# Optimization experiments

Measured on AMD Instinct MI355X. Metric: run time of the kernel, lower is better.

Reference implementation:

```python
import jax, jax.numpy as jnp
import numpy as np

B, T, H, V = 64, 48, 512, 32000


def _uni(k, shape, fan_in):
    s = 1.0 / np.sqrt(fan_in)
    return jax.random.uniform(k, shape, jnp.float32, -s, s)


def setup_inputs() -> dict:
    key = jax.random.key(0)
    ks = jax.random.split(key, 21)
    inp = {
        "feat": jax.random.normal(ks[0], (B, T, H), jnp.float32),
        "caption": jax.random.normal(ks[1], (B, T, H), jnp.float32),
        "ids": jax.random.randint(ks[2], (B, T), 0, V),
    }
    i = 3
    for name, in_dim in (("1", H), ("2", 2 * H), ("d1", H), ("d2", 2 * H)):
        inp["w_ih" + name] = _uni(ks[i], (4 * H, in_dim), H); i += 1
        inp["w_hh" + name] = _uni(ks[i], (4 * H, H), H); i += 1
        inp["b_ih" + name] = _uni(ks[i], (4 * H,), H); i += 1
        inp["b_hh" + name] = _uni(ks[i], (4 * H,), H); i += 1
    inp["w_o"] = _uni(ks[i], (V, H), H); i += 1
    inp["b_o"] = _uni(ks[i], (V,), H)
    return inp


def lstm_cell(x, h, c, w_ih, w_hh, b_ih, b_hh):
    # PyTorch LSTMCell: gates in i, f, g, o order
    g = x @ w_ih.T + b_ih + h @ w_hh.T + b_hh
    gi, gf, gg, go = jnp.split(g, 4, axis=-1)
    c_new = jax.nn.sigmoid(gf) * c + jax.nn.sigmoid(gi) * jnp.tanh(gg)
    h_new = jax.nn.sigmoid(go) * jnp.tanh(c_new)
    return h_new, c_new


def reference(feat, caption, ids,
              w_ih1, w_hh1, b_ih1, b_hh1,
              w_ih2, w_hh2, b_ih2, b_hh2,
              w_ihd1, w_hhd1, b_ihd1, b_hhd1,
              w_ihd2, w_hhd2, b_ihd2, b_hhd2,
              w_o, b_o):
    pad = jnp.zeros((B, H), feat.dtype)
    z = jnp.zeros((B, H), feat.dtype)

    def enc_step(carry, x):
        h1, c1, h2, c2 = carry
        h1, c1 = lstm_cell(x, h1, c1, w_ih1, w_hh1, b_ih1, b_hh1)
        h2, c2 = lstm_cell(jnp.concatenate([pad, h1], 1), h2, c2,
                           w_ih2, w_hh2, b_ih2, b_hh2)
        return (h1, c1, h2, c2), None

    carry, _ = jax.lax.scan(enc_step, (z, z, z, z), jnp.swapaxes(feat, 0, 1))

    def dec_step(carry, xs):
        h1, c1, h2, c2 = carry
        cap, tgt = xs
        h1, c1 = lstm_cell(pad, h1, c1, w_ihd1, w_hhd1, b_ihd1, b_hhd1)
        h2, c2 = lstm_cell(jnp.concatenate([cap, h1], 1), h2, c2,
                           w_ihd2, w_hhd2, b_ihd2, b_hhd2)
        logits = h2 @ w_o.T + b_o  # [B, V]
        lp = jax.nn.log_softmax(logits, axis=-1)
        ce = -jnp.take_along_axis(lp, tgt[:, None], axis=1)[:, 0].mean()
        return (h1, c1, h2, c2), ce

    caps = jnp.swapaxes(caption[:, : T - 1, :], 0, 1)  # [T-1, B, H]
    tgts = jnp.swapaxes(ids[:, 1:T], 0, 1)             # [T-1, B]
    _, ces = jax.lax.scan(dec_step, carry, (caps, tgts))
    # total_loss += sum(mean_ce) / batch_size (word_loss is already a mean)
    return jnp.sum(ces) / B
```

## Files before the change

### kernel.cpp

```cpp
#include <hip/hip_runtime.h>
#include <math.h>

#define B_ 64
#define T_ 48
#define H_ 512
#define V_ 32000
#define G_ 2048
#define BH_ (B_*H_)
#define BG_ (B_*G_)

typedef short short8 __attribute__((ext_vector_type(8)));
typedef float f32x4 __attribute__((ext_vector_type(4)));

__device__ __forceinline__ float sigmoidf_(float x){ return 1.f/(1.f+__expf(-x)); }

__device__ __forceinline__ unsigned short f2bf(float f){
  unsigned u = __float_as_uint(f);
  u += 0x7fffu + ((u>>16)&1u);
  return (unsigned short)(u>>16);
}

__device__ __forceinline__ short8 cvt8(const float* g){
  float4 a = *(const float4*)g;
  float4 b = *(const float4*)(g+4);
  short8 v;
  v[0]=(short)f2bf(a.x); v[1]=(short)f2bf(a.y); v[2]=(short)f2bf(a.z); v[3]=(short)f2bf(a.w);
  v[4]=(short)f2bf(b.x); v[5]=(short)f2bf(b.y); v[6]=(short)f2bf(b.z); v[7]=(short)f2bf(b.w);
  return v;
}

#define F1_(i)   ((i)*16)
#define GO_(i)   ((32+(i))*16)
#define F2_(i)   ((96+(i))*16)
#define GO2_(i)  ((128+(i))*16)

__global__ void init_kernel(unsigned short* h1_0, unsigned short* h2_0, unsigned* flags){
  int i = blockIdx.x*256 + threadIdx.x;
  short8 z = {0,0,0,0,0,0,0,0};
  if (i < 4096) ((short8*)h1_0)[i] = z;
  else          ((short8*)h2_0)[i-4096] = z;
  if (i < 4096) flags[i] = 0u;
}

__global__ void cvt_cat_kernel(const float* __restrict__ s0, int ld0, int off0,
                               const float* __restrict__ s1, int ld1, int off1,
                               unsigned short* __restrict__ dst, int dld, long total8)
{
  int cols8 = dld >> 3;
  for (long i = blockIdx.x*256 + threadIdx.x; i < total8; i += (long)gridDim.x*256){
    int r = (int)(i / cols8);
    int k = (int)(i - (long)r*cols8) * 8;
    short8 v = (k < 512 || !s1) ? cvt8(s0 + (long)r*ld0 + off0 + k)
                                : cvt8(s1 + (long)r*ld1 + off1 + (k-512));
    *(short8*)(dst + (long)r*dld + k) = v;
  }
}

__global__ void bias_sum_kernel(const float* a1, const float* a2, float* o1,
                                const float* b1, const float* b2, float* o2){
  int n = blockIdx.x*256 + threadIdx.x;
  if (n < G_){ o1[n] = a1[n] + a2[n]; o2[n] = b1[n] + b2[n]; }
}

__global__ __launch_bounds__(512,1) void mm_pre_kernel(
    const float* __restrict__ A, int a_bstride,
    const unsigned short* __restrict__ Wbf,
    const float* __restrict__ bA, const float* __restrict__ bB,
    float* __restrict__ out)
{
  const int s = blockIdx.x, n0 = blockIdx.y*256;
  const int t = threadIdx.x, w = t>>6, l = t&63, ln = l&15, lk = l>>4;
  __shared__ short8 smA[64*64];
  __shared__ short8 smB[256*8];

  const float* af32 = A + (long)s*H_;

  f32x4 acc[4][2];
#pragma unroll
  for (int mf=0; mf<4; ++mf)
#pragma unroll
    for (int nf=0; nf<2; ++nf) acc[mf][nf] = (f32x4){0.f,0.f,0.f,0.f};

#pragma unroll
  for (int i=0;i<8;++i){ int e=i*4096+t*8; int m=e>>9, k=e&511;
    smA[m*64 + ((k>>3)^(m&7))] = cvt8(&af32[(long)m*a_bstride + k]); }

  for (int kc=0; kc<8; ++kc){
    __syncthreads();
#pragma unroll
    for (int i=0;i<4;++i){ int e=i*4096+t*8; int n=e>>6, k=e&63;
      smB[n*8 + ((k>>3)^(n&7))] = *(const short8*)(Wbf + (long)(n0+n)*512 + kc*64 + k); }
    __syncthreads();
#pragma unroll
    for (int ks2=0; ks2<2; ++ks2){
#pragma unroll
      for (int nf=0; nf<2; ++nf){
        int n = w*32 + nf*16 + ln;
        short8 bfr = smB[n*8 + ((ks2*4+lk)^(n&7))];
#pragma unroll
        for (int mf=0; mf<4; ++mf){
          int m = mf*16+ln;
          short8 afr = smA[m*64 + (((kc*2+ks2)*4+lk)^(m&7))];
          acc[mf][nf] = __builtin_amdgcn_mfma_f32_16x16x32_bf16(afr, bfr, acc[mf][nf], 0,0,0);
        }
      }
    }
  }
#pragma unroll
  for (int nf=0; nf<2; ++nf){
    int n = n0 + w*32 + nf*16 + ln;
    float bias = bA[n] + bB[n];
#pragma unroll
    for (int mf=0; mf<4; ++mf)
#pragma unroll
      for (int r=0; r<4; ++r){
        int m = mf*16 + lk*4 + r;
        out[(long)s*BG_ + (long)m*G_ + n] = acc[mf][nf][r] + bias;
      }
  }
}

__global__ __launch_bounds__(256,1) void fused_chain_kernel(
    const unsigned short* __restrict__ w1e, const unsigned short* __restrict__ w1d,
    const unsigned short* __restrict__ w2e, const unsigned short* __restrict__ w2d,
    const float* __restrict__ x1,
    const float* __restrict__ capq,
    const float* __restrict__ bd1s, const float* __restrict__ b2es,
    unsigned short* __restrict__ h1, unsigned short* __restrict__ h2,
    unsigned* __restrict__ flags)
{
  const int bc = blockIdx.x;
  const int isL2 = (bc >= 32);
  const int cb = bc & 31;
  const int t = threadIdx.x;
  const int wv = t>>6, l = t&63, ln = l&15, lk = l>>4;

  __shared__ short8 smA[64*128];
  __shared__ float gbuf[4][16][68];
  __shared__ float c_lds[16][68];
  unsigned short* stash = (unsigned short*)&smA[0];

  short8 W[32];
  const int col = wv*512 + cb*16 + ln;
  if (isL2){
    const long wrow = (long)col * 1024;
#pragma unroll
    for (int ks=0; ks<32; ++ks) W[ks] = *(const short8*)(w2e + wrow + ks*32 + lk*8);
  } else {
    const long wrow = (long)col * 512;
#pragma unroll
    for (int ks=0; ks<16; ++ks){
      W[ks]    = *(const short8*)(w1e + wrow + ks*32 + lk*8);
      W[16+ks] = *(const short8*)(w1d + wrow + ks*32 + lk*8);
    }
  }
  const float bext = isL2 ? b2es[col] : bd1s[col];

  for (int i=t; i<16*68; i+=256) (&c_lds[0][0])[i] = 0.f;
  __syncthreads();

  if (!isL2){
    for (int u=0; u<95; ++u){
      float prev[4][4];
      if (u < 48){
        const float* pp = x1 + (long)u*BG_ + col;
#pragma unroll
        for (int mf=0;mf<4;++mf)
#pragma unroll
          for (int r=0;r<4;++r) prev[mf][r] = pp[(long)(mf*16+lk*4+r)*G_];
      } else {
#pragma unroll
        for (int mf=0;mf<4;++mf)
#pragma unroll
          for (int r=0;r<4;++r) prev[mf][r] = bext;
      }
      { const unsigned short* hp = h1 + (long)u*BH_;
#pragma unroll
        for (int i=0;i<16;++i){ int e=i*2048+t*8; int m=e>>9, k=e&511;
          smA[m*128 + ((k>>3)^(m&7))] = *(const short8*)(hp + m*512 + k); } }
      __syncthreads();

      f32x4 acc[4];
#pragma unroll
      for (int mf=0;mf<4;++mf) acc[mf] = (f32x4){0.f,0.f,0.f,0.f};
      if (u < 48){
#pragma unroll
        for (int ks=0; ks<16; ++ks)
#pragma unroll
          for (int mf=0; mf<4; ++mf){
            int m = mf*16+ln;
            acc[mf] = __builtin_amdgcn_mfma_f32_16x16x32_bf16(
              smA[m*128 + ((ks*4+lk)^(m&7))], W[ks], acc[mf], 0,0,0);
          }
      } else {
#pragma unroll
        for (int ks=0; ks<16; ++ks)
#pragma unroll
          for (int mf=0; mf<4; ++mf){
            int m = mf*16+ln;
            acc[mf] = __builtin_amdgcn_mfma_f32_16x16x32_bf16(
              smA[m*128 + ((ks*4+lk)^(m&7))], W[16+ks], acc[mf], 0,0,0);
          }
      }
#pragma unroll
      for (int mf=0;mf<4;++mf)
#pragma unroll
        for (int r=0;r<4;++r) acc[mf][r] += prev[mf][r];

#pragma unroll
      for (int mf=0;mf<4;++mf) *(f32x4*)&gbuf[wv][ln][mf*16+lk*4] = acc[mf];
      __syncthreads();
      {
        int n = t&15, m0 = (t>>4)*4;
        float4 gi = *(float4*)&gbuf[0][n][m0];
        float4 gf = *(float4*)&gbuf[1][n][m0];
        float4 gg = *(float4*)&gbuf[2][n][m0];
        float4 go = *(float4*)&gbuf[3][n][m0];
        float4 c4 = *(float4*)&c_lds[n][m0];
        float cn[4];
        float a_i[4]={gi.x,gi.y,gi.z,gi.w}, a_f[4]={gf.x,gf.y,gf.z,gf.w};
        float a_g[4]={gg.x,gg.y,gg.z,gg.w}, a_o[4]={go.x,go.y,go.z,go.w};
        float ci[4]={c4.x,c4.y,c4.z,c4.w};
#pragma unroll
        for (int j=0;j<4;++j){
          float i_ = sigmoidf_(a_i[j]), f_ = sigmoidf_(a_f[j]), o_ = sigmoidf_(a_o[j]);
          float g_ = tanhf(a_g[j]);
          cn[j] = f_*ci[j] + i_*g_;
          stash[(m0+j)*24 + n] = f2bf(o_*tanhf(cn[j]));
        }
        *(float4*)&c_lds[n][m0] = make_float4(cn[0],cn[1],cn[2],cn[3]);
      }
      __syncthreads();
      {
        unsigned short* ho = h1 + (long)(u+1)*BH_ + cb*16;
        int m = t>>2, q = t&3;
        unsigned long long v = *(const unsigned long long*)&stash[m*24 + q*4];
        __hip_atomic_store((unsigned long long*)(ho + (long)m*512 + q*4), v,
                           __ATOMIC_RELAXED, __HIP_MEMORY_SCOPE_AGENT);
      }
      __syncthreads();

      {
        unsigned g = (unsigned)(u+1);
        if (t == 0)
          __hip_atomic_store(&flags[F1_(cb)], g, __ATOMIC_RELAXED, __HIP_MEMORY_SCOPE_AGENT);
        if (cb == 0){
          if (t < 32)
            while (__hip_atomic_load(&flags[F1_(t)], __ATOMIC_RELAXED, __HIP_MEMORY_SCOPE_AGENT) < g)
              __builtin_amdgcn_s_sleep(1);
          __syncthreads();
          if (t >= 1 && t < 64)
            __hip_atomic_store(&flags[GO_(t)], g, __ATOMIC_RELAXED, __HIP_MEMORY_SCOPE_AGENT);
        } else {
          if (u < 94){
            if (t == 0)
              while (__hip_atomic_load(&flags[GO_(cb)], __ATOMIC_RELAXED, __HIP_MEMORY_SCOPE_AGENT) < g)
                __builtin_amdgcn_s_sleep(1);
          }
          __syncthreads();
        }
      }
    }
  } else {
    for (int v=1; v<=95; ++v){
      if (v == 49){
        const long wrow = (long)col * 1024;
#pragma unroll
        for (int ks=0; ks<32; ++ks) W[ks] = *(const short8*)(w2d + wrow + ks*32 + lk*8);
      }
      int s2 = v-1;
      float prev[4][4];
      if (s2 < 48){
#pragma unroll
        for (int mf=0;mf<4;++mf)
#pragma unroll
          for (int r=0;r<4;++r) prev[mf][r] = bext;
      } else {
        const float* pp = capq + (long)(s2-48)*BG_ + col;
#pragma unroll
        for (int mf=0;mf<4;++mf)
#pragma unroll
          for (int r=0;r<4;++r) prev[mf][r] = pp[(long)(mf*16+lk*4+r)*G_];
      }

      if (t == 0){
        while (__hip_atomic_load(&flags[GO_(bc)], __ATOMIC_RELAXED, __HIP_MEMORY_SCOPE_AGENT) < (unsigned)v)
          __builtin_amdgcn_s_sleep(1);
      }
      __syncthreads();

      { const unsigned short* hpA = h2 + (long)(v-1)*BH_;
        const unsigned short* hpB = h1 + (long)v*BH_;
#pragma unroll
        for (int i=0;i<16;++i){ int e=i*2048+t*8; int m=e>>9, k=e&511;
          smA[m*128 + ((k>>3)^(m&7))]      = *(const short8*)(hpA + m*512 + k);
          smA[m*128 + ((k>>3)^(m&7)) + 64] = *(const short8*)(hpB + m*512 + k);
        } }
      __syncthreads();

      f32x4 acc[4];
#pragma unroll
      for (int mf=0;mf<4;++mf) acc[mf] = (f32x4){0.f,0.f,0.f,0.f};
#pragma unroll
      for (int ks=0; ks<32; ++ks)
#pragma unroll
        for (int mf=0; mf<4; ++mf){
          int m = mf*16+ln;
          acc[mf] = __builtin_amdgcn_mfma_f32_16x16x32_bf16(
            smA[m*128 + ((ks*4+lk)^(m&7))], W[ks], acc[mf], 0,0,0);
        }
#pragma unroll
      for (int mf=0;mf<4;++mf)
#pragma unroll
        for (int r=0;r<4;++r) acc[mf][r] += prev[mf][r];

#pragma unroll
      for (int mf=0;mf<4;++mf) *(f32x4*)&gbuf[wv][ln][mf*16+lk*4] = acc[mf];
      __syncthreads();
      {
        int n = t&15, m0 = (t>>4)*4;
        float4 gi = *(float4*)&gbuf[0][n][m0];
        float4 gf = *(float4*)&gbuf[1][n][m0];
        float4 gg = *(float4*)&gbuf[2][n][m0];
        float4 go = *(float4*)&gbuf[3][n][m0];
        float4 c4 = *(float4*)&c_lds[n][m0];
        float cn[4];
        float a_i[4]={gi.x,gi.y,gi.z,gi.w}, a_f[4]={gf.x,gf.y,gf.z,gf.w};
        float a_g[4]={gg.x,gg.y,gg.z,gg.w}, a_o[4]={go.x,go.y,go.z,go.w};
        float ci[4]={c4.x,c4.y,c4.z,c4.w};
#pragma unroll
        for (int j=0;j<4;++j){
          float i_ = sigmoidf_(a_i[j]), f_ = sigmoidf_(a_f[j]), o_ = sigmoidf_(a_o[j]);
          float g_ = tanhf(a_g[j]);
          cn[j] = f_*ci[j] + i_*g_;
          stash[(m0+j)*24 + n] = f2bf(o_*tanhf(cn[j]));
        }
        *(float4*)&c_lds[n][m0] = make_float4(cn[0],cn[1],cn[2],cn[3]);
      }
      __syncthreads();
      {
        unsigned short* ho = h2 + (long)v*BH_ + cb*16;
        int m = t>>2, q = t&3;
        unsigned long long vv = *(const unsigned long long*)&stash[m*24 + q*4];
        __hip_atomic_store((unsigned long long*)(ho + (long)m*512 + q*4), vv,
                           __ATOMIC_RELAXED, __HIP_MEMORY_SCOPE_AGENT);
      }
      __syncthreads();

      if (v < 95){
        unsigned g = (unsigned)v;
        if (t == 0)
          __hip_atomic_store(&flags[F2_(cb)], g, __ATOMIC_RELAXED, __HIP_MEMORY_SCOPE_AGENT);
        if (cb == 0){
          if (t < 32)
            while (__hip_atomic_load(&flags[F2_(t)], __ATOMIC_RELAXED, __HIP_MEMORY_SCOPE_AGENT) < g)
              __builtin_amdgcn_s_sleep(1);
          __syncthreads();
          if (t >= 1 && t < 32)
            __hip_atomic_store(&flags[GO2_(t)], g, __ATOMIC_RELAXED, __HIP_MEMORY_SCOPE_AGENT);
        } else {
          if (t == 0)
            while (__hip_atomic_load(&flags[GO2_(cb)], __ATOMIC_RELAXED, __HIP_MEMORY_SCOPE_AGENT) < g)
              __builtin_amdgcn_s_sleep(1);
          __syncthreads();
        }
      }
    }
  }
}

__global__ __launch_bounds__(512,1) void ce_mfma_kernel(
    const unsigned short* __restrict__ h2_bf, const unsigned short* __restrict__ wo_bf,
    const float* __restrict__ b_o, const int* __restrict__ ids,
    float* __restrict__ partial, float* __restrict__ tgt)
{
  const int td = blockIdx.x, vt = blockIdx.y, v0 = vt*256;
  const int t = threadIdx.x, w = t>>6, l = t&63, ln = l&15, lk = l>>4;
  __shared__ short8 smA[64*64];
  __shared__ short8 smB[256*8];
  __shared__ float red[8][64];
  __shared__ int tid_s[64];

  const unsigned short* hp = h2_bf + (long)(49+td)*BH_;
  if (t < 64) tid_s[t] = ids[t*T_ + td + 1];
#pragma unroll
  for (int i=0;i<8;++i){ int e=i*4096+t*8; int m=e>>9, k=e&511;
    smA[m*64 + ((k>>3)^(m&7))] = *(const short8*)(hp + m*512 + k); }

  f32x4 acc[4][2];
#pragma unroll
  for (int mf=0; mf<4; ++mf)
#pragma unroll
    for (int nf=0; nf<2; ++nf) acc[mf][nf] = (f32x4){0.f,0.f,0.f,0.f};

  for (int kc=0; kc<8; ++kc){
    __syncthreads();
#pragma unroll
    for (int i=0;i<4;++i){ int e=i*4096+t*8; int n=e>>6, k=e&63;
      smB[n*8 + ((k>>3)^(n&7))] = *(const short8*)(wo_bf + (long)(v0+n)*512 + kc*64 + k); }
    __syncthreads();
#pragma unroll
    for (int ks2=0; ks2<2; ++ks2){
#pragma unroll
      for (int nf=0; nf<2; ++nf){
        int n = w*32 + nf*16 + ln;
        short8 bfr = smB[n*8 + ((ks2*4+lk)^(n&7))];
#pragma unroll
        for (int mf=0; mf<4; ++mf){
          int m = mf*16+ln;
          short8 afr = smA[m*64 + (((kc*2+ks2)*4+lk)^(m&7))];
          acc[mf][nf] = __builtin_amdgcn_mfma_f32_16x16x32_bf16(afr, bfr, acc[mf][nf], 0,0,0);
        }
      }
    }
  }

  float se[4][4];
#pragma unroll
  for (int mf=0; mf<4; ++mf)
#pragma unroll
    for (int r=0;r<4;++r) se[mf][r] = 0.f;
#pragma unroll
  for (int nf=0; nf<2; ++nf){
    int ng = v0 + w*32 + nf*16 + ln;
    float bo = b_o[ng];
#pragma unroll
    for (int mf=0; mf<4; ++mf)
#pragma unroll
      for (int r=0;r<4;++r){
        int m = mf*16 + lk*4 + r;
        float lg = acc[mf][nf][r] + bo;
        se[mf][r] += __expf(lg);
        if (ng == tid_s[m]) tgt[td*64 + m] = lg;
      }
  }
#pragma unroll
  for (int off=1; off<16; off<<=1)
#pragma unroll
    for (int mf=0; mf<4; ++mf)
#pragma unroll
      for (int r=0;r<4;++r) se[mf][r] += __shfl_xor(se[mf][r], off);
  if (ln == 0){
#pragma unroll
    for (int mf=0; mf<4; ++mf)
      *(f32x4*)&red[w][mf*16 + lk*4] = (f32x4){se[mf][0],se[mf][1],se[mf][2],se[mf][3]};
  }
  __syncthreads();
  if (t < 64){
    float ssum = 0.f;
#pragma unroll
    for (int w2=0; w2<8; ++w2) ssum += red[w2][t];
    partial[(long)vt*3008 + td*64 + t] = ssum;
  }
}

__global__ void ce_combine(const float* __restrict__ partial, const float* __restrict__ tgt,
                           float* __restrict__ ce_row){
  int r = blockIdx.x*256 + threadIdx.x;
  if (r < 3008){
    float s = 0.f;
    for (int i=0;i<125;++i) s += partial[(long)i*3008 + r];
    ce_row[r] = __logf(s) - tgt[r];
  }
}

__global__ void ce_final(const float* __restrict__ ce_row, float* __restrict__ out){
  __shared__ float red[256];
  float s = 0.f;
  for (int i=threadIdx.x; i<3008; i+=256) s += ce_row[i];
  red[threadIdx.x] = s;
  __syncthreads();
  for (int off=128; off>0; off>>=1){
    if (threadIdx.x < off) red[threadIdx.x] += red[threadIdx.x + off];
    __syncthreads();
  }
  if (threadIdx.x == 0) out[0] = red[0] * (1.0f/4096.0f);
}

extern "C" void kernel_launch(void* const* d_in, const int* in_sizes, int n_in,
                              void* d_out, int out_size, void* d_ws, size_t ws_size,
                              hipStream_t stream)
{
  (void)in_sizes; (void)n_in; (void)out_size; (void)ws_size;
  const float* feat    = (const float*)d_in[0];
  const float* caption = (const float*)d_in[1];
  const int*   ids     = (const int*)d_in[2];
  const float* w_ih1  = (const float*)d_in[3];
  const float* w_hh1  = (const float*)d_in[4];
  const float* b_ih1  = (const float*)d_in[5];
  const float* b_hh1  = (const float*)d_in[6];
  const float* w_ih2  = (const float*)d_in[7];
  const float* w_hh2  = (const float*)d_in[8];
  const float* b_ih2  = (const float*)d_in[9];
  const float* b_hh2  = (const float*)d_in[10];
  const float* w_hhd1 = (const float*)d_in[12];
  const float* b_ihd1 = (const float*)d_in[13];
  const float* b_hhd1 = (const float*)d_in[14];
  const float* w_ihd2 = (const float*)d_in[15];
  const float* w_hhd2 = (const float*)d_in[16];
  const float* b_ihd2 = (const float*)d_in[17];
  const float* b_hhd2 = (const float*)d_in[18];
  const float* w_o    = (const float*)d_in[19];
  const float* b_o    = (const float*)d_in[20];

  char* p = (char*)d_ws;
  unsigned short* h1   = (unsigned short*)p; p += 96L*BH_*2;
  unsigned short* h2   = (unsigned short*)p; p += 96L*BH_*2;
  unsigned short* w1e  = (unsigned short*)p; p += 2048L*512*2;
  unsigned short* w1d  = (unsigned short*)p; p += 2048L*512*2;
  unsigned short* w2e  = (unsigned short*)p; p += 2048L*1024*2;
  unsigned short* w2d  = (unsigned short*)p; p += 2048L*1024*2;
  unsigned short* wx1  = (unsigned short*)p; p += 2048L*512*2;
  unsigned short* wcap = (unsigned short*)p; p += 2048L*512*2;
  float* x1    = (float*)p;
  unsigned short* wo_bf = (unsigned short*)p;
  p += 48L*BG_*4;
  float* capq  = (float*)p; p += 47L*BG_*4;
  float* bd1s  = (float*)p; p += 2048*4;
  float* b2es  = (float*)p; p += 2048*4;
  float* partial = (float*)p; p += 125L*3008*4;
  float* tgt   = (float*)p; p += 3008*4;
  float* ce_row= (float*)p; p += 3008*4;
  unsigned* flags = (unsigned*)p; p += 4096*4;

  init_kernel<<<32, 256, 0, stream>>>(h1, h2, flags);

  cvt_cat_kernel<<<256, 256, 0, stream>>>(w_hh1, 512, 0, nullptr, 0, 0, w1e, 512, 2048L*64);
  cvt_cat_kernel<<<256, 256, 0, stream>>>(w_hhd1, 512, 0, nullptr, 0, 0, w1d, 512, 2048L*64);
  cvt_cat_kernel<<<256, 256, 0, stream>>>(w_hh2, 512, 0, w_ih2, 1024, 512, w2e, 1024, 2048L*128);
  cvt_cat_kernel<<<256, 256, 0, stream>>>(w_hhd2, 512, 0, w_ihd2, 1024, 512, w2d, 1024, 2048L*128);
  cvt_cat_kernel<<<256, 256, 0, stream>>>(w_ih1, 512, 0, nullptr, 0, 0, wx1, 512, 2048L*64);
  cvt_cat_kernel<<<256, 256, 0, stream>>>(w_ihd2, 1024, 0, nullptr, 0, 0, wcap, 512, 2048L*64);
  bias_sum_kernel<<<8, 256, 0, stream>>>(b_ihd1, b_hhd1, bd1s, b_ih2, b_hh2, b2es);

  mm_pre_kernel<<<dim3(48,8), 512, 0, stream>>>(feat, T_*H_, wx1, b_ih1, b_hh1, x1);
  mm_pre_kernel<<<dim3(47,8), 512, 0, stream>>>(caption, T_*H_, wcap, b_ihd2, b_hhd2, capq);

  fused_chain_kernel<<<64, 256, 0, stream>>>(w1e, w1d, w2e, w2d, x1, capq, bd1s, b2es, h1, h2, flags);

  cvt_cat_kernel<<<512, 256, 0, stream>>>(w_o, 512, 0, nullptr, 0, 0, wo_bf, 512, 32000L*64);

  ce_mfma_kernel<<<dim3(47,125), 512, 0, stream>>>(h2, wo_bf, b_o, ids, partial, tgt);
  ce_combine<<<12, 256, 0, stream>>>(partial, tgt, ce_row);
  ce_final<<<1, 256, 0, stream>>>(ce_row, (float*)d_out);
}
```

Before: 1.593 ms.

## Fuse LSTM layers into shared blocks and overlap output-projection CE with recurrence

Merges the two LSTM layers into the same 32 blocks: each block now computes layer 1 at step u and layer 2 at step u-1 in one iteration, which removes the separate layer-2 grid barrier. It adds 208 persistent blocks that wait on per-step flags and run the vocab projection and softmax partial sums as soon as each decoder h2 is ready, so the cross-entropy work overlaps the serial recurrence. These blocks convert w_o from fp32 on the fly, and the precomputed input projections are stored as bf16. The cost is more per-step work and register pressure in the recurrent blocks, repeated fp32 weight loads in the CE path, and reliance on spin-wait co-residency of 240 blocks.

Result: slower. 1.846 ms (+15.9%).

```diff
diff --git a/kernel.cpp b/kernel.cpp
--- a/kernel.cpp
+++ b/kernel.cpp
@@ -8,6 +8,7 @@
 #define G_ 2048
 #define BH_ (B_*H_)
 #define BG_ (B_*G_)
+#define NCE_ 208
 
 typedef short short8 __attribute__((ext_vector_type(8)));
 typedef float f32x4 __attribute__((ext_vector_type(4)));
@@ -18,6 +19,9 @@
   unsigned u = __float_as_uint(f);
   u += 0x7fffu + ((u>>16)&1u);
   return (unsigned short)(u>>16);
+}
+__device__ __forceinline__ float bf2f(unsigned short u){
+  return __uint_as_float(((unsigned)u)<<16);
 }
 
 __device__ __forceinline__ short8 cvt8(const float* g){
@@ -31,15 +35,14 @@
 
 #define F1_(i)   ((i)*16)
 #define GO_(i)   ((32+(i))*16)
-#define F2_(i)   ((96+(i))*16)
-#define GO2_(i)  ((128+(i))*16)
+#define CEGO_(i) ((64+(i))*16)
 
 __global__ void init_kernel(unsigned short* h1_0, unsigned short* h2_0, unsigned* flags){
   int i = blockIdx.x*256 + threadIdx.x;
   short8 z = {0,0,0,0,0,0,0,0};
   if (i < 4096) ((short8*)h1_0)[i] = z;
   else          ((short8*)h2_0)[i-4096] = z;
-  if (i < 4096) flags[i] = 0u;
+  if (i < 4352) flags[i] = 0u;
 }
 
 __global__ void cvt_cat_kernel(const float* __restrict__ s0, int ld0, int off0,
@@ -66,7 +69,7 @@
     const float* __restrict__ A, int a_bstride,
     const unsigned short* __restrict__ Wbf,
     const float* __restrict__ bA, const float* __restrict__ bB,
-    float* __restrict__ out)
+    unsigned short* __restrict__ out)
 {
   const int s = blockIdx.x, n0 = blockIdx.y*256;
   const int t = threadIdx.x, w = t>>6, l = t&63, ln = l&15, lk = l>>4;
@@ -115,112 +118,164 @@
 #pragma unroll
       for (int r=0; r<4; ++r){
         int m = mf*16 + lk*4 + r;
-        out[(long)s*BG_ + (long)m*G_ + n] = acc[mf][nf][r] + bias;
+        out[(long)s*BG_ + (long)m*G_ + n] = f2bf(acc[mf][nf][r] + bias);
       }
   }
 }
 
-__global__ __launch_bounds__(256,1) void fused_chain_kernel(
+__global__ __launch_bounds__(256,1) void mega_kernel(
     const unsigned short* __restrict__ w1e, const unsigned short* __restrict__ w1d,
     const unsigned short* __restrict__ w2e, const unsigned short* __restrict__ w2d,
-    const float* __restrict__ x1,
-    const float* __restrict__ capq,
+    const unsigned short* __restrict__ x1b,
+    const unsigned short* __restrict__ capqb,
     const float* __restrict__ bd1s, const float* __restrict__ b2es,
     unsigned short* __restrict__ h1, unsigned short* __restrict__ h2,
+    const float* __restrict__ w_o, const float* __restrict__ b_o, const int* __restrict__ ids,
+    float* __restrict__ partial, float* __restrict__ tgt,
     unsigned* __restrict__ flags)
 {
+  __shared__ short8 smA[64*128];
+  __shared__ float gbuf[4][16][68];
+  __shared__ float c1_lds[16][68];
+  __shared__ float c2_lds[16][68];
   const int bc = blockIdx.x;
-  const int isL2 = (bc >= 32);
-  const int cb = bc & 31;
   const int t = threadIdx.x;
   const int wv = t>>6, l = t&63, ln = l&15, lk = l>>4;
 
-  __shared__ short8 smA[64*128];
-  __shared__ float gbuf[4][16][68];
-  __shared__ float c_lds[16][68];
-  unsigned short* stash = (unsigned short*)&smA[0];
-
-  short8 W[32];
-  const int col = wv*512 + cb*16 + ln;
-  if (isL2){
-    const long wrow = (long)col * 1024;
-#pragma unroll
-    for (int ks=0; ks<32; ++ks) W[ks] = *(const short8*)(w2e + wrow + ks*32 + lk*8);
-  } else {
-    const long wrow = (long)col * 512;
-#pragma unroll
-    for (int ks=0; ks<16; ++ks){
-      W[ks]    = *(const short8*)(w1e + wrow + ks*32 + lk*8);
-      W[16+ks] = *(const short8*)(w1d + wrow + ks*32 + lk*8);
+  if (bc < 32){
+    const int cb = bc;
+    unsigned short* stash = (unsigned short*)&smA[0];
+    short8 W1e_[16], W1d_[16], W2_[32];
+    const int col = wv*512 + cb*16 + ln;
+    {
+      const long wr1 = (long)col * 512;
+#pragma unroll
+      for (int ks=0; ks<16; ++ks){
+        W1e_[ks] = *(const short8*)(w1e + wr1 + ks*32 + lk*8);
+        W1d_[ks] = *(const short8*)(w1d + wr1 + ks*32 + lk*8);
+      }
+      const long wr2 = (long)col * 1024;
+#pragma unroll
+      for (int ks=0; ks<32; ++ks)
+        W2_[ks] = *(const short8*)(w2e + wr2 + ks*32 + lk*8);
     }
-  }
-  const float bext = isL2 ? b2es[col] : bd1s[col];
-
-  for (int i=t; i<16*68; i+=256) (&c_lds[0][0])[i] = 0.f;
-  __syncthreads();
-
-  if (!isL2){
-    for (int u=0; u<95; ++u){
-      float prev[4][4];
-      if (u < 48){
-        const float* pp = x1 + (long)u*BG_ + col;
+    const float b1d = bd1s[col], b2e = b2es[col];
+
+    for (int i=t; i<16*68; i+=256){ (&c1_lds[0][0])[i] = 0.f; (&c2_lds[0][0])[i] = 0.f; }
+    __syncthreads();
+
+    for (int u=0; u<96; ++u){
+      if (u == 49){
+        const long wr2 = (long)col * 1024;
+#pragma unroll
+        for (int ks=0; ks<32; ++ks)
+          W2_[ks] = *(const short8*)(w2d + wr2 + ks*32 + lk*8);
+      }
+      const int L1a = (u<=94), L2a = (u>=1);
+
+      float prev1[4][4], prev2[4][4];
+      if (L1a){
+        if (u < 48){
+          const unsigned short* pp = x1b + (long)u*BG_ + col;
+#pragma unroll
+          for (int mf=0;mf<4;++mf)
+#pragma unroll
+            for (int r=0;r<4;++r) prev1[mf][r] = bf2f(pp[(long)(mf*16+lk*4+r)*G_]);
+        } else {
+#pragma unroll
+          for (int mf=0;mf<4;++mf)
+#pragma unroll
+            for (int r=0;r<4;++r) prev1[mf][r] = b1d;
+        }
+      }
+      if (L2a){
+        if (u-1 < 48){
+#pragma unroll
+          for (int mf=0;mf<4;++mf)
+#pragma unroll
+            for (int r=0;r<4;++r) prev2[mf][r] = b2e;
+        } else {
+          const unsigned short* pp = capqb + (long)(u-1-48)*BG_ + col;
+#pragma unroll
+          for (int mf=0;mf<4;++mf)
+#pragma unroll
+            for (int r=0;r<4;++r) prev2[mf][r] = bf2f(pp[(long)(mf*16+lk*4+r)*G_]);
+        }
+      }
+
+      { const unsigned short* hpB = h1 + (long)u*BH_;
+#pragma unroll
+        for (int i=0;i<16;++i){ int e=i*2048+t*8; int m=e>>9, k=e&511;
+          smA[m*128 + ((k>>3)^(m&7)) + 64] = *(const short8*)(hpB + m*512 + k); }
+        if (L2a){
+          const unsigned short* hpA = h2 + (long)(u-1)*BH_;
+#pragma unroll
+          for (int i=0;i<16;++i){ int e=i*2048+t*8; int m=e>>9, k=e&511;
+            smA[m*128 + ((k>>3)^(m&7))] = *(const short8*)(hpA + m*512 + k); }
+        }
+      }
+      __syncthreads();
+
+      f32x4 acc1[4], acc2[4];
+      if (L1a){
+#pragma unroll
+        for (int mf=0;mf<4;++mf) acc1[mf] = (f32x4){0.f,0.f,0.f,0.f};
+        if (u < 48){
+#pragma unroll
+          for (int ks=0; ks<16; ++ks)
+#pragma unroll
+            for (int mf=0; mf<4; ++mf){
+              int m = mf*16+ln;
+              acc1[mf] = __builtin_amdgcn_mfma_f32_16x16x32_bf16(
+                smA[m*128 + 64 + ((ks*4+lk)^(m&7))], W1e_[ks], acc1[mf], 0,0,0);
+            }
+        } else {
+#pragma unroll
+          for (int ks=0; ks<16; ++ks)
+#pragma unroll
+            for (int mf=0; mf<4; ++mf){
+              int m = mf*16+ln;
+              acc1[mf] = __builtin_amdgcn_mfma_f32_16x16x32_bf16(
+                smA[m*128 + 64 + ((ks*4+lk)^(m&7))], W1d_[ks], acc1[mf], 0,0,0);
+            }
+        }
 #pragma unroll
         for (int mf=0;mf<4;++mf)
 #pragma unroll
-          for (int r=0;r<4;++r) prev[mf][r] = pp[(long)(mf*16+lk*4+r)*G_];
-      } else {
-#pragma unroll
-        for (int mf=0;mf<4;++mf)
-#pragma unroll
-          for (int r=0;r<4;++r) prev[mf][r] = bext;
-      }
-      { const unsigned short* hp = h1 + (long)u*BH_;
-#pragma unroll
-        for (int i=0;i<16;++i){ int e=i*2048+t*8; int m=e>>9, k=e&511;
-          smA[m*128 + ((k>>3)^(m&7))] = *(const short8*)(hp + m*512 + k); } }
-      __syncthreads();
-
-      f32x4 acc[4];
-#pragma unroll
-      for (int mf=0;mf<4;++mf) acc[mf] = (f32x4){0.f,0.f,0.f,0.f};
-      if (u < 48){
-#pragma unroll
-        for (int ks=0; ks<16; ++ks)
+          for (int r=0;r<4;++r) acc1[mf][r] += prev1[mf][r];
+      }
+      if (L2a){
+#pragma unroll
+        for (int mf=0;mf<4;++mf) acc2[mf] = (f32x4){0.f,0.f,0.f,0.f};
+#pragma unroll
+        for (int ks=0; ks<32; ++ks)
 #pragma unroll
           for (int mf=0; mf<4; ++mf){
             int m = mf*16+ln;
-            acc[mf] = __builtin_amdgcn_mfma_f32_16x16x32_bf16(
-              smA[m*128 + ((ks*4+lk)^(m&7))], W[ks], acc[mf], 0,0,0);
+            acc2[mf] = __builtin_amdgcn_mfma_f32_16x16x32_bf16(
+              smA[m*128 + ((ks*4+lk)^(m&7))], W2_[ks], acc2[mf], 0,0,0);
           }
-      } else {
-#pragma unroll
-        for (int ks=0; ks<16; ++ks)
-#pragma unroll
-          for (int mf=0; mf<4; ++mf){
-            int m = mf*16+ln;
-            acc[mf] = __builtin_amdgcn_mfma_f32_16x16x32_bf16(
-              smA[m*128 + ((ks*4+lk)^(m&7))], W[16+ks], acc[mf], 0,0,0);
-          }
-      }
-#pragma unroll
-      for (int mf=0;mf<4;++mf)
-#pragma unroll
-        for (int r=0;r<4;++r) acc[mf][r] += prev[mf][r];
-
-#pragma unroll
-      for (int mf=0;mf<4;++mf) *(f32x4*)&gbuf[wv][ln][mf*16+lk*4] = acc[mf];
-      __syncthreads();
-      {
+#pragma unroll
+        for (int mf=0;mf<4;++mf)
+#pragma unroll
+          for (int r=0;r<4;++r) acc2[mf][r] += prev2[mf][r];
+      }
+
+      if (L1a){
+#pragma unroll
+        for (int mf=0;mf<4;++mf) *(f32x4*)&gbuf[wv][ln][mf*16+lk*4] = acc1[mf];
+      }
+      __syncthreads();
+      if (L1a){
         int n = t&15, m0 = (t>>4)*4;
         float4 gi = *(float4*)&gbuf[0][n][m0];
         float4 gf = *(float4*)&gbuf[1][n][m0];
         float4 gg = *(float4*)&gbuf[2][n][m0];
         float4 go = *(float4*)&gbuf[3][n][m0];
-        float4 c4 = *(float4*)&c_lds[n][m0];
-        float cn[4];
+        float4 c4 = *(float4*)&c1_lds[n][m0];
         float a_i[4]={gi.x,gi.y,gi.z,gi.w}, a_f[4]={gf.x,gf.y,gf.z,gf.w};
         float a_g[4]={gg.x,gg.y,gg.z,gg.w}, a_o[4]={go.x,go.y,go.z,go.w};
-        float ci[4]={c4.x,c4.y,c4.z,c4.w};
+        float ci[4]={c4.x,c4.y,c4.z,c4.w}, cn[4];
 #pragma unroll
         for (int j=0;j<4;++j){
           float i_ = sigmoidf_(a_i[j]), f_ = sigmoidf_(a_f[j]), o_ = sigmoidf_(a_o[j]);
@@ -228,10 +283,10 @@
           cn[j] = f_*ci[j] + i_*g_;
           stash[(m0+j)*24 + n] = f2bf(o_*tanhf(cn[j]));
         }
-        *(float4*)&c_lds[n][m0] = make_float4(cn[0],cn[1],cn[2],cn[3]);
-      }
-      __syncthreads();
-      {
+        *(float4*)&c1_lds[n][m0] = make_float4(cn[0],cn[1],cn[2],cn[3]);
+      }
+      __syncthreads();
+      if (L1a){
         unsigned short* ho = h1 + (long)(u+1)*BH_ + cb*16;
         int m = t>>2, q = t&3;
         unsigned long long v = *(const unsigned long long*)&stash[m*24 + q*4];
@@ -240,8 +295,42 @@
       }
       __syncthreads();
 
+      if (L2a){
+#pragma unroll
+        for (int mf=0;mf<4;++mf) *(f32x4*)&gbuf[wv][ln][mf*16+lk*4] = acc2[mf];
+      }
+      __syncthreads();
+      if (L2a){
+        int n = t&15, m0 = (t>>4)*4;
+        float4 gi = *(float4*)&gbuf[0][n][m0];
+        float4 gf = *(float4*)&gbuf[1][n][m0];
+        float4 gg = *(float4*)&gbuf[2][n][m0];
+        float4 go = *(float4*)&gbuf[3][n][m0];
+        float4 c4 = *(float4*)&c2_lds[n][m0];
+        float a_i[4]={gi.x,gi.y,gi.z,gi.w}, a_f[4]={gf.x,gf.y,gf.z,gf.w};
+        float a_g[4]={gg.x,gg.y,gg.z,gg.w}, a_o[4]={go.x,go.y,go.z,go.w};
+        float ci[4]={c4.x,c4.y,c4.z,c4.w}, cn[4];
+#pragma unroll
+        for (int j=0;j<4;++j){
+          float i_ = sigmoidf_(a_i[j]), f_ = sigmoidf_(a_f[j]), o_ = sigmoidf_(a_o[j]);
+          float g_ = tanhf(a_g[j]);
+          cn[j] = f_*ci[j] + i_*g_;
+          stash[(m0+j)*24 + n] = f2bf(o_*tanhf(cn[j]));
+        }
+        *(float4*)&c2_lds[n][m0] = make_float4(cn[0],cn[1],cn[2],cn[3]);
+      }
+      __syncthreads();
+      if (L2a){
+        unsigned short* ho = h2 + (long)u*BH_ + cb*16;
+        int m = t>>2, q = t&3;
+        unsigned long long v = *(const unsigned long long*)&stash[m*24 + q*4];
+        __hip_atomic_store((unsigned long long*)(ho + (long)m*512 + q*4), v,
+                           __ATOMIC_RELAXED, __HIP_MEMORY_SCOPE_AGENT);
+      }
+
       {
         unsigned g = (unsigned)(u+1);
+        __syncthreads();
         if (t == 0)
           __hip_atomic_store(&flags[F1_(cb)], g, __ATOMIC_RELAXED, __HIP_MEMORY_SCOPE_AGENT);
         if (cb == 0){
@@ -249,10 +338,12 @@
             while (__hip_atomic_load(&flags[F1_(t)], __ATOMIC_RELAXED, __HIP_MEMORY_SCOPE_AGENT) < g)
               __builtin_amdgcn_s_sleep(1);
           __syncthreads();
-          if (t >= 1 && t < 64)
+          if (t >= 1 && t < 32)
             __hip_atomic_store(&flags[GO_(t)], g, __ATOMIC_RELAXED, __HIP_MEMORY_SCOPE_AGENT);
+          else if (t >= 32 && t < 32+NCE_)
+            __hip_atomic_store(&flags[CEGO_(t-32)], g, __ATOMIC_RELAXED, __HIP_MEMORY_SCOPE_AGENT);
         } else {
-          if (u < 94){
+          if (u < 95){
             if (t == 0)
               while (__hip_atomic_load(&flags[GO_(cb)], __ATOMIC_RELAXED, __HIP_MEMORY_SCOPE_AGENT) < g)
                 __builtin_amdgcn_s_sleep(1);
@@ -262,195 +353,91 @@
       }
     }
   } else {
-    for (int v=1; v<=95; ++v){
-      if (v == 49){
-        const long wrow = (long)col * 1024;
-#pragma unroll
-        for (int ks=0; ks<32; ++ks) W[ks] = *(const short8*)(w2d + wrow + ks*32 + lk*8);
-      }
-      int s2 = v-1;
-      float prev[4][4];
-      if (s2 < 48){
-#pragma unroll
-        for (int mf=0;mf<4;++mf)
-#pragma unroll
-          for (int r=0;r<4;++r) prev[mf][r] = bext;
-      } else {
-        const float* pp = capq + (long)(s2-48)*BG_ + col;
-#pragma unroll
-        for (int mf=0;mf<4;++mf)
-#pragma unroll
-          for (int r=0;r<4;++r) prev[mf][r] = pp[(long)(mf*16+lk*4+r)*G_];
-      }
-
+    const int ceid = bc - 32;
+    short8* smB = (short8*)&gbuf[0][0][0];
+    float (*red)[64] = (float(*)[64])&c1_lds[0][0];
+    int* tid_s = (int*)&c2_lds[0][0];
+
+    for (int g2 = ceid; g2 < 47*250; g2 += NCE_){
+      int td = g2 / 250, vt = g2 - td*250, v0 = vt*128;
       if (t == 0){
-        while (__hip_atomic_load(&flags[GO_(bc)], __ATOMIC_RELAXED, __HIP_MEMORY_SCOPE_AGENT) < (unsigned)v)
-          __builtin_amdgcn_s_sleep(1);
-      }
-      __syncthreads();
-
-      { const unsigned short* hpA = h2 + (long)(v-1)*BH_;
-        const unsigned short* hpB = h1 + (long)v*BH_;
+        unsigned need = (unsigned)(50 + td);
+        while (__hip_atomic_load(&flags[CEGO_(ceid)], __ATOMIC_RELAXED, __HIP_MEMORY_SCOPE_AGENT) < need)
+          __builtin_amdgcn_s_sleep(8);
+      }
+      __syncthreads();
+
+      if (t < 64) tid_s[t] = ids[t*T_ + td + 1];
+      { const unsigned short* hp = h2 + (long)(49+td)*BH_;
 #pragma unroll
         for (int i=0;i<16;++i){ int e=i*2048+t*8; int m=e>>9, k=e&511;
-          smA[m*128 + ((k>>3)^(m&7))]      = *(const short8*)(hpA + m*512 + k);
-          smA[m*128 + ((k>>3)^(m&7)) + 64] = *(const short8*)(hpB + m*512 + k);
-        } }
-      __syncthreads();
-
-      f32x4 acc[4];
-#pragma unroll
-      for (int mf=0;mf<4;++mf) acc[mf] = (f32x4){0.f,0.f,0.f,0.f};
-#pragma unroll
-      for (int ks=0; ks<32; ++ks)
-#pragma unroll
-        for (int mf=0; mf<4; ++mf){
-          int m = mf*16+ln;
-          acc[mf] = __builtin_amdgcn_mfma_f32_16x16x32_bf16(
-            smA[m*128 + ((ks*4+lk)^(m&7))], W[ks], acc[mf], 0,0,0);
-        }
-#pragma unroll
-      for (int mf=0;mf<4;++mf)
-#pragma unroll
-        for (int r=0;r<4;++r) acc[mf][r] += prev[mf][r];
-
-#pragma unroll
-      for (int mf=0;mf<4;++mf) *(f32x4*)&gbuf[wv][ln][mf*16+lk*4] = acc[mf];
-      __syncthreads();
-      {
-        int n = t&15, m0 = (t>>4)*4;
-        float4 gi = *(float4*)&gbuf[0][n][m0];
-        float4 gf = *(float4*)&gbuf[1][n][m0];
-        float4 gg = *(float4*)&gbuf[2][n][m0];
-        float4 go = *(float4*)&gbuf[3][n][m0];
-        float4 c4 = *(float4*)&c_lds[n][m0];
-        float cn[4];
-        float a_i[4]={gi.x,gi.y,gi.z,gi.w}, a_f[4]={gf.x,gf.y,gf.z,gf.w};
-        float a_g[4]={gg.x,gg.y,gg.z,gg.w}, a_o[4]={go.x,go.y,go.z,go.w};
-        float ci[4]={c4.x,c4.y,c4.z,c4.w};
-#pragma unroll
-        for (int j=0;j<4;++j){
-          float i_ = sigmoidf_(a_i[j]), f_ = sigmoidf_(a_f[j]), o_ = sigmoidf_(a_o[j]);
-          float g_ = tanhf(a_g[j]);
-          cn[j] = f_*ci[j] + i_*g_;
-          stash[(m0+j)*24 + n] = f2bf(o_*tanhf(cn[j]));
-        }
-        *(float4*)&c_lds[n][m0] = make_float4(cn[0],cn[1],cn[2],cn[3]);
-      }
-      __syncthreads();
-      {
-        unsigned short* ho = h2 + (long)v*BH_ + cb*16;
-        int m = t>>2, q = t&3;
-        unsigned long long vv = *(const unsigned long long*)&stash[m*24 + q*4];
-        __hip_atomic_store((unsigned long long*)(ho + (long)m*512 + q*4), vv,
-                           __ATOMIC_RELAXED, __HIP_MEMORY_SCOPE_AGENT);
-      }
-      __syncthreads();
-
-      if (v < 95){
-        unsigned g = (unsigned)v;
-        if (t == 0)
-          __hip_atomic_store(&flags[F2_(cb)], g, __ATOMIC_RELAXED, __HIP_MEMORY_SCOPE_AGENT);
-        if (cb == 0){
-          if (t < 32)
-            while (__hip_atomic_load(&flags[F2_(t)], __ATOMIC_RELAXED, __HIP_MEMORY_SCOPE_AGENT) < g)
-              __builtin_amdgcn_s_sleep(1);
-          __syncthreads();
-          if (t >= 1 && t < 32)
-            __hip_atomic_store(&flags[GO2_(t)], g, __ATOMIC_RELAXED, __HIP_MEMORY_SCOPE_AGENT);
-        } else {
-          if (t == 0)
-            while (__hip_atomic_load(&flags[GO2_(cb)], __ATOMIC_RELAXED, __HIP_MEMORY_SCOPE_AGENT) < g)
-              __builtin_amdgcn_s_sleep(1);
-          __syncthreads();
-        }
-      }
+          smA[m*64 + ((k>>3)^(m&7))] = *(const short8*)(hp + m*512 + k); } }
+
+      f32x4 acc[4][2];
+#pragma unroll
+      for (int mf=0; mf<4; ++mf)
+#pragma unroll
+        for (int nf=0; nf<2; ++nf) acc[mf][nf] = (f32x4){0.f,0.f,0.f,0.f};
+
+      for (int kc=0; kc<8; ++kc){
+        __syncthreads();
+#pragma unroll
+        for (int i=0;i<4;++i){ int e=i*2048+t*8; int n=e>>6, k=e&63;
+          smB[n*8 + ((k>>3)^(n&7))] = cvt8(&w_o[(long)(v0+n)*512 + kc*64 + k]); }
+        __syncthreads();
+#pragma unroll
+        for (int ks2=0; ks2<2; ++ks2){
+#pragma unroll
+          for (int nf=0; nf<2; ++nf){
+            int n = wv*32 + nf*16 + ln;
+            short8 bfr = smB[n*8 + ((ks2*4+lk)^(n&7))];
+#pragma unroll
+            for (int mf=0; mf<4; ++mf){
+              int m = mf*16+ln;
+              short8 afr = smA[m*64 + (((kc*2+ks2)*4+lk)^(m&7))];
+              acc[mf][nf] = __builtin_amdgcn_mfma_f32_16x16x32_bf16(afr, bfr, acc[mf][nf], 0,0,0);
+            }
+          }
+        }
+      }
+
+      float se[4][4];
+#pragma unroll
+      for (int mf=0; mf<4; ++mf)
+#pragma unroll
+        for (int r=0;r<4;++r) se[mf][r] = 0.f;
+#pragma unroll
+      for (int nf=0; nf<2; ++nf){
+        int ng = v0 + wv*32 + nf*16 + ln;
+        float bo = b_o[ng];
+#pragma unroll
+        for (int mf=0; mf<4; ++mf)
+#pragma unroll
+          for (int r=0;r<4;++r){
+            int m = mf*16 + lk*4 + r;
+            float lg = acc[mf][nf][r] + bo;
+            se[mf][r] += __expf(lg);
+            if (ng == tid_s[m]) tgt[td*64 + m] = lg;
+          }
+      }
+#pragma unroll
+      for (int off=1; off<16; off<<=1)
+#pragma unroll
+        for (int mf=0; mf<4; ++mf)
+#pragma unroll
+          for (int r=0;r<4;++r) se[mf][r] += __shfl_xor(se[mf][r], off);
+      if (ln == 0){
+#pragma unroll
+        for (int mf=0; mf<4; ++mf)
+          *(f32x4*)&red[wv][mf*16 + lk*4] = (f32x4){se[mf][0],se[mf][1],se[mf][2],se[mf][3]};
+      }
+      __syncthreads();
+      if (t < 64){
+        float ssum = red[0][t] + red[1][t] + red[2][t] + red[3][t];
+        partial[(long)vt*3008 + td*64 + t] = ssum;
+      }
+      __syncthreads();
     }
-  }
-}
-
-__global__ __launch_bounds__(512,1) void ce_mfma_kernel(
-    const unsigned short* __restrict__ h2_bf, const unsigned short* __restrict__ wo_bf,
-    const float* __restrict__ b_o, const int* __restrict__ ids,
-    float* __restrict__ partial, float* __restrict__ tgt)
-{
-  const int td = blockIdx.x, vt = blockIdx.y, v0 = vt*256;
-  const int t = threadIdx.x, w = t>>6, l = t&63, ln = l&15, lk = l>>4;
-  __shared__ short8 smA[64*64];
-  __shared__ short8 smB[256*8];
-  __shared__ float red[8][64];
-  __shared__ int tid_s[64];
-
-  const unsigned short* hp = h2_bf + (long)(49+td)*BH_;
-  if (t < 64) tid_s[t] = ids[t*T_ + td + 1];
-#pragma unroll
-  for (int i=0;i<8;++i){ int e=i*4096+t*8; int m=e>>9, k=e&511;
-    smA[m*64 + ((k>>3)^(m&7))] = *(const short8*)(hp + m*512 + k); }
-
-  f32x4 acc[4][2];
-#pragma unroll
-  for (int mf=0; mf<4; ++mf)
-#pragma unroll
-    for (int nf=0; nf<2; ++nf) acc[mf][nf] = (f32x4){0.f,0.f,0.f,0.f};
-
-  for (int kc=0; kc<8; ++kc){
-    __syncthreads();
-#pragma unroll
-    for (int i=0;i<4;++i){ int e=i*4096+t*8; int n=e>>6, k=e&63;
-      smB[n*8 + ((k>>3)^(n&7))] = *(const short8*)(wo_bf + (long)(v0+n)*512 + kc*64 + k); }
-    __syncthreads();
-#pragma unroll
-    for (int ks2=0; ks2<2; ++ks2){
-#pragma unroll
-      for (int nf=0; nf<2; ++nf){
-        int n = w*32 + nf*16 + ln;
-        short8 bfr = smB[n*8 + ((ks2*4+lk)^(n&7))];
-#pragma unroll
-        for (int mf=0; mf<4; ++mf){
-          int m = mf*16+ln;
-          short8 afr = smA[m*64 + (((kc*2+ks2)*4+lk)^(m&7))];
-          acc[mf][nf] = __builtin_amdgcn_mfma_f32_16x16x32_bf16(afr, bfr, acc[mf][nf], 0,0,0);
-        }
-      }
-    }
-  }
-
-  float se[4][4];
-#pragma unroll
-  for (int mf=0; mf<4; ++mf)
-#pragma unroll
-    for (int r=0;r<4;++r) se[mf][r] = 0.f;
-#pragma unroll
-  for (int nf=0; nf<2; ++nf){
-    int ng = v0 + w*32 + nf*16 + ln;
-    float bo = b_o[ng];
-#pragma unroll
-    for (int mf=0; mf<4; ++mf)
-#pragma unroll
-      for (int r=0;r<4;++r){
-        int m = mf*16 + lk*4 + r;
-        float lg = acc[mf][nf][r] + bo;
-        se[mf][r] += __expf(lg);
-        if (ng == tid_s[m]) tgt[td*64 + m] = lg;
-      }
-  }
-#pragma unroll
-  for (int off=1; off<16; off<<=1)
-#pragma unroll
-    for (int mf=0; mf<4; ++mf)
-#pragma unroll
-      for (int r=0;r<4;++r) se[mf][r] += __shfl_xor(se[mf][r], off);
-  if (ln == 0){
-#pragma unroll
-    for (int mf=0; mf<4; ++mf)
-      *(f32x4*)&red[w][mf*16 + lk*4] = (f32x4){se[mf][0],se[mf][1],se[mf][2],se[mf][3]};
-  }
-  __syncthreads();
-  if (t < 64){
-    float ssum = 0.f;
-#pragma unroll
-    for (int w2=0; w2<8; ++w2) ssum += red[w2][t];
-    partial[(long)vt*3008 + td*64 + t] = ssum;
   }
 }
 
@@ -459,7 +446,7 @@
   int r = blockIdx.x*256 + threadIdx.x;
   if (r < 3008){
     float s = 0.f;
-    for (int i=0;i<125;++i) s += partial[(long)i*3008 + r];
+    for (int i=0;i<250;++i) s += partial[(long)i*3008 + r];
     ce_row[r] = __logf(s) - tgt[r];
   }
 }
@@ -504,24 +491,22 @@
   const float* b_o    = (const float*)d_in[20];
 
   char* p = (char*)d_ws;
-  unsigned short* h1   = (unsigned short*)p; p += 96L*BH_*2;
-  unsigned short* h2   = (unsigned short*)p; p += 96L*BH_*2;
-  unsigned short* w1e  = (unsigned short*)p; p += 2048L*512*2;
-  unsigned short* w1d  = (unsigned short*)p; p += 2048L*512*2;
-  unsigned short* w2e  = (unsigned short*)p; p += 2048L*1024*2;
-  unsigned short* w2d  = (unsigned short*)p; p += 2048L*1024*2;
-  unsigned short* wx1  = (unsigned short*)p; p += 2048L*512*2;
-  unsigned short* wcap = (unsigned short*)p; p += 2048L*512*2;
-  float* x1    = (float*)p;
-  unsigned short* wo_bf = (unsigned short*)p;
-  p += 48L*BG_*4;
-  float* capq  = (float*)p; p += 47L*BG_*4;
+  unsigned short* h1    = (unsigned short*)p; p += 96L*BH_*2;
+  unsigned short* h2    = (unsigned short*)p; p += 96L*BH_*2;
+  unsigned short* w1e   = (unsigned short*)p; p += 2048L*512*2;
+  unsigned short* w1d   = (unsigned short*)p; p += 2048L*512*2;
+  unsigned short* w2e   = (unsigned short*)p; p += 2048L*1024*2;
+  unsigned short* w2d   = (unsigned short*)p; p += 2048L*1024*2;
+  unsigned short* wx1   = (unsigned short*)p; p += 2048L*512*2;
+  unsigned short* wcap  = (unsigned short*)p; p += 2048L*512*2;
+  unsigned short* x1b   = (unsigned short*)p; p += 48L*BG_*2;
+  unsigned short* capqb = (unsigned short*)p; p += 47L*BG_*2;
   float* bd1s  = (float*)p; p += 2048*4;
   float* b2es  = (float*)p; p += 2048*4;
-  float* partial = (float*)p; p += 125L*3008*4;
+  float* partial = (float*)p; p += 250L*3008*4;
   float* tgt   = (float*)p; p += 3008*4;
   float* ce_row= (float*)p; p += 3008*4;
-  unsigned* flags = (unsigned*)p; p += 4096*4;
+  unsigned* flags = (unsigned*)p; p += 4352*4;
 
   init_kernel<<<32, 256, 0, stream>>>(h1, h2, flags);
 
@@ -533,14 +518,13 @@
   cvt_cat_kernel<<<256, 256, 0, stream>>>(w_ihd2, 1024, 0, nullptr, 0, 0, wcap, 512, 2048L*64);
   bias_sum_kernel<<<8, 256, 0, stream>>>(b_ihd1, b_hhd1, bd1s, b_ih2, b_hh2, b2es);
 
-  mm_pre_kernel<<<dim3(48,8), 512, 0, stream>>>(feat, T_*H_, wx1, b_ih1, b_hh1, x1);
-  mm_pre_kernel<<<dim3(47,8), 512, 0, stream>>>(caption, T_*H_, wcap, b_ihd2, b_hhd2, capq);
-
-  fused_chain_kernel<<<64, 256, 0, stream>>>(w1e, w1d, w2e, w2d, x1, capq, bd1s, b2es, h1, h2, flags);
-
-  cvt_cat_kernel<<<512, 256, 0, stream>>>(w_o, 512, 0, nullptr, 0, 0, wo_bf, 512, 32000L*64);
-
-  ce_mfma_kernel<<<dim3(47,125), 512, 0, stream>>>(h2, wo_bf, b_o, ids, partial, tgt);
+  mm_pre_kernel<<<dim3(48,8), 512, 0, stream>>>(feat, T_*H_, wx1, b_ih1, b_hh1, x1b);
+  mm_pre_kernel<<<dim3(47,8), 512, 0, stream>>>(caption, T_*H_, wcap, b_ihd2, b_hhd2, capqb);
+
+  mega_kernel<<<32+NCE_, 256, 0, stream>>>(
+      w1e, w1d, w2e, w2d, x1b, capqb, bd1s, b2es, h1, h2,
+      w_o, b_o, ids, partial, tgt, flags);
+
   ce_combine<<<12, 256, 0, stream>>>(partial, tgt, ce_row);
   ce_final<<<1, 256, 0, stream>>>(ce_row, (float*)d_out);
 }
```
